# Optimization experiments

Measured on AMD Instinct MI355X. Metric: run time of the kernel, lower is better.

Reference implementation:

```python
import jax, jax.numpy as jnp
import numpy as np

NUM_KNNS = 200
TEMPERATURE = 0.07
NUM_CLASSES = 1000


def setup_inputs() -> dict:
    key = jax.random.key(0)
    k1, k2, k3, k4 = jax.random.split(key, 4)
    N, D, K = 1024, 512, 65536
    # features and queue are L2-normalized (queue init is normal_l2)
    features = jax.random.normal(k1, (N, D), jnp.float32)
    features = features / jnp.linalg.norm(features, axis=-1, keepdims=True)
    queue_features = jax.random.normal(k2, (K, D), jnp.float32)
    queue_features = queue_features / jnp.linalg.norm(queue_features, axis=-1, keepdims=True)
    labels = jax.random.randint(k3, (N,), 0, NUM_CLASSES, dtype=jnp.int32)
    queue_labels = jax.random.randint(k4, (K,), 0, NUM_CLASSES, dtype=jnp.int32)
    return {
        "features": features,
        "queue_features": queue_features,
        "labels": labels,
        "queue_labels": queue_labels,
        "queue_ptr": 0,
    }


def reference(features, queue_features, labels, queue_labels, queue_ptr):
    # --- kNN accuracy ---
    # similarity matmul: [N, K]
    sim = jnp.einsum('nd,kd->nk', features, queue_features)
    sim_weight, sim_indices = jax.lax.top_k(sim, k=NUM_KNNS)  # [N, k]
    sim_weight = jnp.exp(sim_weight / TEMPERATURE)
    # gather neighbor labels (equivalent to the one-hot einsum in the original)
    sim_labels = queue_labels[sim_indices]  # [N, k] int32
    one_hot_labels = jax.nn.one_hot(sim_labels, NUM_CLASSES, dtype=sim_weight.dtype)  # [N, k, C]
    pred_scores = jnp.sum(one_hot_labels * sim_weight[..., None], axis=1)  # [N, C]
    pred_labels = jnp.argmax(pred_scores, axis=-1)
    accuracy = jnp.mean((pred_labels == labels).astype(jnp.float32))

    # --- circular queue scatter update ---
    N = features.shape[0]
    K = queue_features.shape[0]
    inds = jnp.arange(N) + queue_ptr
    new_queue_features = queue_features.at[inds].set(features)
    new_queue_labels = queue_labels.at[inds].set(labels)
    new_queue_ptr = (queue_ptr + N) % K
    return accuracy, new_queue_features, new_queue_labels, new_queue_ptr
```

## Files before the change

kernel.cpp:

```cpp
#include <hip/hip_runtime.h>
#include <math.h>

#define N_ROWS 1024
#define DIM    512
#define KQ     65536
#define KNN    200
#define NCLS   1000
#define NBINS  4096
#define CAP    2048
#define INV_T  14.285714285714286f

typedef unsigned short u16;
typedef __attribute__((ext_vector_type(8))) short short8;
typedef __attribute__((ext_vector_type(4))) float f32x4;
struct alignas(8) U16x4 { u16 x, y, z, w; };

#define GLOAD_LDS16(g, l)                                               \
    __builtin_amdgcn_global_load_lds(                                   \
        (__attribute__((address_space(1))) void*)(g),                   \
        (__attribute__((address_space(3))) void*)(l), 16, 0, 0)

__device__ __forceinline__ void split1(float x, u16& h, u16& l) {
    unsigned u = __float_as_uint(x);
    unsigned hr = (u + 0x7FFFu + ((u >> 16) & 1u)) >> 16;
    float hf = __uint_as_float(hr << 16);
    float lo = x - hf;
    unsigned ul = __float_as_uint(lo);
    unsigned lr = (ul + 0x7FFFu + ((ul >> 16) & 1u)) >> 16;
    h = (u16)hr; l = (u16)lr;
}

#define QF_BLOCKS (KQ * DIM / 4 / 256)
#define FT_BLOCKS (N_ROWS * DIM / 4 / 256)

__global__ __launch_bounds__(256) void fused_update_split_kernel(
    const float* __restrict__ feats, const float* __restrict__ qf,
    const int* __restrict__ labels, const int* __restrict__ ql,
    const int* __restrict__ qptr,
    float* __restrict__ out_qf, float* __restrict__ out_ql,
    float* __restrict__ out_ptr,
    u16* __restrict__ Bhi, u16* __restrict__ Blo,
    u16* __restrict__ Ahi, u16* __restrict__ Alo) {
    int ptr = qptr[0];
    int b = blockIdx.x;
    if (b < QF_BLOCKS) {
        size_t t = (size_t)b * 256 + threadIdx.x;
        size_t idx = t * 4;
        int row = (int)(idx >> 9);
        int col = (int)(idx & 511);
        float4 v = *(const float4*)(qf + idx);
        U16x4 h, l;
        split1(v.x, h.x, l.x); split1(v.y, h.y, l.y);
        split1(v.z, h.z, l.z); split1(v.w, h.w, l.w);
        *(U16x4*)(Bhi + idx) = h;
        *(U16x4*)(Blo + idx) = l;
        int d = row - ptr; if (d < 0) d += KQ;
        float4 o = (d < N_ROWS) ? *(const float4*)(feats + (size_t)d * DIM + col) : v;
        *(float4*)(out_qf + idx) = o;
        if (col == 0)
            out_ql[row] = (float)((d < N_ROWS) ? labels[d] : ql[row]);
    } else {
        size_t t = (size_t)(b - QF_BLOCKS) * 256 + threadIdx.x;
        size_t idx = t * 4;
        float4 v = *(const float4*)(feats + idx);
        U16x4 h, l;
        split1(v.x, h.x, l.x); split1(v.y, h.y, l.y);
        split1(v.z, h.z, l.z); split1(v.w, h.w, l.w);
        *(U16x4*)(Ahi + idx) = h;
        *(U16x4*)(Alo + idx) = l;
        if (t == 0) out_ptr[0] = (float)((ptr + N_ROWS) % KQ);
    }
}

__global__ __launch_bounds__(256, 4) void gemm_mfma_kernel(
    const u16* __restrict__ Ahi, const u16* __restrict__ Alo,
    const u16* __restrict__ Bhi, const u16* __restrict__ Blo,
    float* __restrict__ C) {
    __shared__ u16 sA[2][128 * 32];
    __shared__ u16 sB[2][128 * 32];

    int tid = threadIdx.x;
    int wave = tid >> 6, lane = tid & 63;
    int q = lane >> 4, r = lane & 15;
    int bn = blockIdx.x, bm = blockIdx.y;
    int wm = wave & 1, wn = wave >> 1;

    const u16* gplane = (wave == 0) ? Ahi : (wave == 1) ? Alo
                      : (wave == 2) ? Bhi : Blo;
    int prow0 = (wave < 2) ? bm * 128 : bn * 128;
    const u16* gbase = gplane + (size_t)prow0 * DIM;
    u16* lbase = (wave == 0) ? sA[0] : (wave == 1) ? sA[1]
               : (wave == 2) ? sB[0] : sB[1];
    int lrow = lane >> 2;
    int lchunk = lane & 3;

    f32x4 acc[4][4] = {};

    for (int kt = 0; kt < DIM; kt += 32) {
        __syncthreads();
#pragma unroll
        for (int s = 0; s < 8; ++s) {
            const u16* g = gbase + (size_t)(s * 16 + lrow) * DIM + kt + lchunk * 8;
            GLOAD_LDS16(g, lbase + s * 512);
        }
        __syncthreads();

        short8 fa[2][4], fb[2][4];
#pragma unroll
        for (int t = 0; t < 4; ++t) {
            int am = wm * 64 + t * 16 + r;
            fa[0][t] = *(const short8*)&sA[0][am * 32 + q * 8];
            fa[1][t] = *(const short8*)&sA[1][am * 32 + q * 8];
            int bn_ = wn * 64 + t * 16 + r;
            fb[0][t] = *(const short8*)&sB[0][bn_ * 32 + q * 8];
            fb[1][t] = *(const short8*)&sB[1][bn_ * 32 + q * 8];
        }
#pragma unroll
        for (int i = 0; i < 4; ++i)
#pragma unroll
            for (int j = 0; j < 4; ++j) {
                acc[i][j] = __builtin_amdgcn_mfma_f32_16x16x32_bf16(
                    fa[0][i], fb[0][j], acc[i][j], 0, 0, 0);
                acc[i][j] = __builtin_amdgcn_mfma_f32_16x16x32_bf16(
                    fa[0][i], fb[1][j], acc[i][j], 0, 0, 0);
                acc[i][j] = __builtin_amdgcn_mfma_f32_16x16x32_bf16(
                    fa[1][i], fb[0][j], acc[i][j], 0, 0, 0);
            }
    }

#pragma unroll
    for (int i = 0; i < 4; ++i)
#pragma unroll
        for (int j = 0; j < 4; ++j)
#pragma unroll
            for (int g = 0; g < 4; ++g) {
                int row = bm * 128 + wm * 64 + i * 16 + q * 4 + g;
                int col = bn * 128 + wn * 64 + j * 16 + r;
                C[(size_t)row * KQ + col] = acc[i][j][g];
            }
}

#define LSTR 68
#define LA(k, m) ((k) * LSTR + (m))

__global__ __launch_bounds__(256) void gemm_nt_kernel(
    const float* __restrict__ A, const float* __restrict__ B,
    float* __restrict__ C) {
    __shared__ float As[32 * LSTR];
    __shared__ float Bs[32 * LSTR];
    int tid = threadIdx.x;
    int bn = blockIdx.x, bm = blockIdx.y;
    int tx = tid & 15, ty = tid >> 4;
    int lm = tid >> 3;
    int lk = (tid & 7) * 4;
    const float* Ab = A + (size_t)bm * 64 * DIM;
    const float* Bb = B + (size_t)bn * 64 * DIM;
    float acc[4][4] = {};
    for (int kt = 0; kt < DIM; kt += 32) {
        float4 a0 = *(const float4*)(Ab + (size_t)lm * DIM + kt + lk);
        float4 a1 = *(const float4*)(Ab + (size_t)(lm + 32) * DIM + kt + lk);
        float4 b0 = *(const float4*)(Bb + (size_t)lm * DIM + kt + lk);
        float4 b1 = *(const float4*)(Bb + (size_t)(lm + 32) * DIM + kt + lk);
        __syncthreads();
        As[LA(lk + 0, lm)] = a0.x;  As[LA(lk + 1, lm)] = a0.y;
        As[LA(lk + 2, lm)] = a0.z;  As[LA(lk + 3, lm)] = a0.w;
        As[LA(lk + 0, lm + 32)] = a1.x;  As[LA(lk + 1, lm + 32)] = a1.y;
        As[LA(lk + 2, lm + 32)] = a1.z;  As[LA(lk + 3, lm + 32)] = a1.w;
        Bs[LA(lk + 0, lm)] = b0.x;  Bs[LA(lk + 1, lm)] = b0.y;
        Bs[LA(lk + 2, lm)] = b0.z;  Bs[LA(lk + 3, lm)] = b0.w;
        Bs[LA(lk + 0, lm + 32)] = b1.x;  Bs[LA(lk + 1, lm + 32)] = b1.y;
        Bs[LA(lk + 2, lm + 32)] = b1.z;  Bs[LA(lk + 3, lm + 32)] = b1.w;
        __syncthreads();
#pragma unroll
        for (int kk = 0; kk < 32; ++kk) {
            float4 av = *(const float4*)&As[LA(kk, ty * 4)];
            float4 bv = *(const float4*)&Bs[LA(kk, tx * 4)];
            float a_[4] = {av.x, av.y, av.z, av.w};
            float b_[4] = {bv.x, bv.y, bv.z, bv.w};
#pragma unroll
            for (int i = 0; i < 4; ++i)
#pragma unroll
                for (int j = 0; j < 4; ++j) acc[i][j] += a_[i] * b_[j];
        }
    }
    for (int i = 0; i < 4; ++i) {
        float4 o = make_float4(acc[i][0], acc[i][1], acc[i][2], acc[i][3]);
        *(float4*)(C + (size_t)(bm * 64 + ty * 4 + i) * KQ + bn * 64 + tx * 4) = o;
    }
}

__device__ __forceinline__ unsigned order_key(float v) {
    unsigned u = __float_as_uint(v);
    return u ^ ((u & 0x80000000u) ? 0xFFFFFFFFu : 0x80000000u);
}

__global__ __launch_bounds__(1024) void topk_kernel(
    const float* __restrict__ sim, int r0,
    const int* __restrict__ ql, const int* __restrict__ labels,
    float* __restrict__ flags) {
    __shared__ unsigned hist[NBINS];
    __shared__ unsigned psum[1024];
    __shared__ float cval[CAP];
    __shared__ int   cidx[CAP];
    __shared__ float scores[NCLS];
    __shared__ float rbest[1024];
    __shared__ int   rcls[1024];
    __shared__ int   s_bstar, s_ncand;

    int row = blockIdx.x;
    int tid = threadIdx.x;
    const float4* s4 = (const float4*)(sim + (size_t)row * KQ);

    hist[tid] = 0; hist[tid + 1024] = 0; hist[tid + 2048] = 0; hist[tid + 3072] = 0;
    if (tid == 0) s_ncand = 0;
    __syncthreads();

    for (int i4 = tid; i4 < KQ / 4; i4 += 1024) {
        float4 v = s4[i4];
        atomicAdd(&hist[order_key(v.x) >> 20], 1u);
        atomicAdd(&hist[order_key(v.y) >> 20], 1u);
        atomicAdd(&hist[order_key(v.z) >> 20], 1u);
        atomicAdd(&hist[order_key(v.w) >> 20], 1u);
    }
    __syncthreads();

    unsigned loc = hist[4 * tid] + hist[4 * tid + 1] +
                   hist[4 * tid + 2] + hist[4 * tid + 3];
    psum[tid] = loc;
    __syncthreads();
    for (int off = 1; off < 1024; off <<= 1) {
        unsigned add = (tid + off < 1024) ? psum[tid + off] : 0u;
        __syncthreads();
        psum[tid] += add;
        __syncthreads();
    }
    unsigned running = psum[tid] - loc;
    for (int j = 3; j >= 0; --j) {
        unsigned c = hist[4 * tid + j];
        if (running < KNN && running + c >= KNN) s_bstar = 4 * tid + j;
        running += c;
    }
    __syncthreads();
    int bstar = s_bstar;

    for (int i4 = tid; i4 < KQ / 4; i4 += 1024) {
        float4 v = s4[i4];
        float vv[4] = {v.x, v.y, v.z, v.w};
#pragma unroll
        for (int c = 0; c < 4; ++c) {
            if ((int)(order_key(vv[c]) >> 20) >= bstar) {
                int p = atomicAdd(&s_ncand, 1);
                if (p < CAP) { cval[p] = vv[c]; cidx[p] = i4 * 4 + c; }
            }
        }
    }
    if (tid < NCLS) scores[tid] = 0.f;
    __syncthreads();

    int M = s_ncand; if (M > CAP) M = CAP;
    for (int c = tid; c < M; c += 1024) {
        float v = cval[c]; int id = cidx[c];
        int rank = 0;
        for (int j = 0; j < M; ++j) {
            float vj = cval[j];
            if (vj > v || (vj == v && cidx[j] < id)) rank++;
        }
        if (rank < KNN) {
            float w = expf(v * INV_T);
            atomicAdd(&scores[ql[id]], w);
        }
    }
    __syncthreads();

    float best = -1.f; int bc = 0;
    if (tid < NCLS) { best = scores[tid]; bc = tid; }
    rbest[tid] = best; rcls[tid] = bc;
    __syncthreads();
    for (int off = 512; off; off >>= 1) {
        if (tid < off) {
            float ob = rbest[tid + off]; int oc = rcls[tid + off];
            if (ob > rbest[tid] || (ob == rbest[tid] && oc < rcls[tid])) {
                rbest[tid] = ob; rcls[tid] = oc;
            }
        }
        __syncthreads();
    }
    if (tid == 0)
        flags[r0 + row] = (rcls[0] == labels[r0 + row]) ? 1.0f : 0.0f;
}

__global__ __launch_bounds__(256) void acc_kernel(
    const float* __restrict__ flags, float* __restrict__ out) {
    __shared__ float r[256];
    int tid = threadIdx.x;
    r[tid] = flags[tid] + flags[tid + 256] + flags[tid + 512] + flags[tid + 768];
    __syncthreads();
    for (int off = 128; off; off >>= 1) {
        if (tid < off) r[tid] += r[tid + off];
        __syncthreads();
    }
    if (tid == 0) out[0] = r[0] * (1.0f / 1024.0f);
}

extern "C" void kernel_launch(void* const* d_in, const int* in_sizes, int n_in,
                              void* d_out, int out_size, void* d_ws, size_t ws_size,
                              hipStream_t stream) {
    const float* feats  = (const float*)d_in[0];
    const float* qf     = (const float*)d_in[1];
    const int*   labels = (const int*)d_in[2];
    const int*   ql     = (const int*)d_in[3];
    const int*   qptr   = (const int*)d_in[4];

    float* out     = (float*)d_out;
    float* out_qf  = out + 1;
    float* out_ql  = out_qf + (size_t)KQ * DIM;
    float* out_ptr = out_ql + KQ;

    const size_t bplane = (size_t)KQ * DIM;
    const size_t aplane = (size_t)N_ROWS * DIM;

    int CH = 0;
    for (int c = 256; c >= 128; c >>= 1) {
        size_t need = 2 * bplane * 2 + 2 * aplane * 2 +
                      (size_t)c * KQ * 4 + N_ROWS * 4;
        if (need <= ws_size) { CH = c; break; }
    }

    if (CH > 0) {
        u16* Bhi = (u16*)d_ws;
        u16* Blo = Bhi + bplane;
        u16* Ahi = Blo + bplane;
        u16* Alo = Ahi + aplane;
        float* sim   = (float*)(Alo + aplane);
        float* flags = sim + (size_t)CH * KQ;

        fused_update_split_kernel<<<QF_BLOCKS + FT_BLOCKS, 256, 0, stream>>>(
            feats, qf, labels, ql, qptr, out_qf, out_ql, out_ptr,
            Bhi, Blo, Ahi, Alo);

        int nchunks = N_ROWS / CH;
        for (int c = 0; c < nchunks; ++c) {
            dim3 g(KQ / 128, CH / 128);
            gemm_mfma_kernel<<<g, 256, 0, stream>>>(
                Ahi + (size_t)c * CH * DIM, Alo + (size_t)c * CH * DIM,
                Bhi, Blo, sim);
            topk_kernel<<<CH, 1024, 0, stream>>>(sim, c * CH, ql, labels, flags);
        }
        acc_kernel<<<1, 256, 0, stream>>>(flags, out);
    } else {
        int CHf = 256;
        while (CHf > 64 &&
               ((size_t)CHf * KQ * sizeof(float) + N_ROWS * sizeof(float)) > ws_size)
            CHf >>= 1;
        float* sim   = (float*)d_ws;
        float* flags = (float*)((char*)d_ws + (size_t)CHf * KQ * sizeof(float));
        fused_update_split_kernel<<<QF_BLOCKS + FT_BLOCKS, 256, 0, stream>>>(
            feats, qf, labels, ql, qptr, out_qf, out_ql, out_ptr,
            (u16*)sim, (u16*)sim, (u16*)sim, (u16*)sim);
        int nchunks = N_ROWS / CHf;
        for (int c = 0; c < nchunks; ++c) {
            const float* A = feats + (size_t)c * CHf * DIM;
            dim3 g(KQ / 64, CHf / 64);
            gemm_nt_kernel<<<g, 256, 0, stream>>>(A, qf, sim);
            topk_kernel<<<CHf, 1024, 0, stream>>>(sim, c * CHf, ql, labels, flags);
        }
        acc_kernel<<<1, 256, 0, stream>>>(flags, out);
    }
}
```

Baseline: 669.5 us.

## Add 256x256-tile split-bf16 MFMA GEMM with ping-pong LDS staging and priority scheduling

Adds a new GEMM kernel for the split-bf16 (hi/lo) similarity matmul that uses 256x256 output tiles with 512 threads and 8 waves. It double-buffers LDS via direct global-to-LDS loads, interleaves fragment loads and MFMA groups with barriers and s_setprio, and walks 24 k-steps covering the three hi/lo plane products. The goal is more data reuse per LDS load and better overlap of memory with MFMA than the 128x128 kernel. It only runs when the chunk size is 256, and the large register and LDS footprint could limit occupancy.

After: 611.9 us. -8.6%, faster.

```diff
diff --git a/kernel.cpp b/kernel.cpp
--- a/kernel.cpp
+++ b/kernel.cpp
@@ -72,6 +72,129 @@
     }
 }
 
+#define NKT 24
+
+#define STAGE8(kt_, dA, dB)                                                    \
+  {                                                                            \
+    const u16* Ap_ = ((kt_) < 16) ? Ahi : Alo;                                 \
+    const u16* Bp_ = (((kt_) >> 3) == 1) ? Blo : Bhi;                          \
+    int ke_ = ((kt_) & 7) << 6;                                                \
+    const u16* ga_ = Ap_ + (size_t)(r0A + srow) * DIM + ke_ + scol;            \
+    const u16* gb_ = Bp_ + (size_t)(r0B + srow) * DIM + ke_ + scol;            \
+    GLOAD_LDS16(ga_ + (size_t)(8 * w0) * DIM,         &dA[0][w0 * 512]);       \
+    GLOAD_LDS16(ga_ + (size_t)(8 * w1) * DIM,         &dA[0][w1 * 512]);       \
+    GLOAD_LDS16(ga_ + (size_t)(128 + 8 * w0) * DIM,   &dA[1][w0 * 512]);       \
+    GLOAD_LDS16(ga_ + (size_t)(128 + 8 * w1) * DIM,   &dA[1][w1 * 512]);       \
+    GLOAD_LDS16(gb_ + (size_t)(8 * w0) * DIM,         &dB[0][w0 * 512]);       \
+    GLOAD_LDS16(gb_ + (size_t)(8 * w1) * DIM,         &dB[0][w1 * 512]);       \
+    GLOAD_LDS16(gb_ + (size_t)(128 + 8 * w0) * DIM,   &dB[1][w0 * 512]);       \
+    GLOAD_LDS16(gb_ + (size_t)(128 + 8 * w1) * DIM,   &dB[1][w1 * 512]);       \
+  }
+
+#define MM(t_, u_)                                                             \
+  acc[t_][u_] = __builtin_amdgcn_mfma_f32_16x16x32_bf16(                       \
+      fa[(t_) & 3][0], fb[u_][0], acc[t_][u_], 0, 0, 0);                       \
+  acc[t_][u_] = __builtin_amdgcn_mfma_f32_16x16x32_bf16(                       \
+      fa[(t_) & 3][1], fb[u_][1], acc[t_][u_], 0, 0, 0);
+
+#define TILE(kt_, RA, RB, SA, SB, DO_STAGE)                                    \
+  {                                                                            \
+    asm volatile("s_waitcnt vmcnt(0)" ::: "memory");                           \
+    __builtin_amdgcn_s_barrier();                                              \
+    const u16* aH_ = &RA[wm][0];                                               \
+    const u16* bH_ = &RB[wn >> 1][bB];                                         \
+                                                                  \
+    _Pragma("unroll") for (int t = 0; t < 4; ++t) {                            \
+      fa[t][0] = *(const short8*)(aH_ + t * 1024 + aoff + c0);                 \
+      fa[t][1] = *(const short8*)(aH_ + t * 1024 + aoff + c1);                 \
+    }                                                                          \
+    _Pragma("unroll") for (int u = 0; u < 2; ++u) {                            \
+      fb[u][0] = *(const short8*)(bH_ + u * 1024 + aoff + c0);                 \
+      fb[u][1] = *(const short8*)(bH_ + u * 1024 + aoff + c1);                 \
+    }                                                                          \
+    if (DO_STAGE) STAGE8((kt_) + 1, SA, SB);                                   \
+    __builtin_amdgcn_s_barrier();                                              \
+    __builtin_amdgcn_s_setprio(1);                                             \
+    _Pragma("unroll") for (int t = 0; t < 4; ++t) {                            \
+      MM(t, 0); MM(t, 1);                                                      \
+    }                                                                          \
+    __builtin_amdgcn_s_setprio(0);                                             \
+    __builtin_amdgcn_s_barrier();                                              \
+                                                                  \
+    _Pragma("unroll") for (int u = 2; u < 4; ++u) {                            \
+      fb[u][0] = *(const short8*)(bH_ + u * 1024 + aoff + c0);                 \
+      fb[u][1] = *(const short8*)(bH_ + u * 1024 + aoff + c1);                 \
+    }                                                                          \
+    __builtin_amdgcn_s_barrier();                                              \
+    __builtin_amdgcn_s_setprio(1);                                             \
+    _Pragma("unroll") for (int t = 0; t < 4; ++t) {                            \
+      MM(t, 2); MM(t, 3);                                                      \
+    }                                                                          \
+    __builtin_amdgcn_s_setprio(0);                                             \
+    __builtin_amdgcn_s_barrier();                                              \
+                                                                  \
+    _Pragma("unroll") for (int t = 0; t < 4; ++t) {                            \
+      fa[t][0] = *(const short8*)(aH_ + (t + 4) * 1024 + aoff + c0);           \
+      fa[t][1] = *(const short8*)(aH_ + (t + 4) * 1024 + aoff + c1);           \
+    }                                                                          \
+    __builtin_amdgcn_s_barrier();                                              \
+    __builtin_amdgcn_s_setprio(1);                                             \
+    _Pragma("unroll") for (int t = 4; t < 8; ++t) {                            \
+      MM(t, 2); MM(t, 3);                                                      \
+    }                                                                          \
+    __builtin_amdgcn_s_setprio(0);                                             \
+    __builtin_amdgcn_s_barrier();                                              \
+                                                                  \
+    __builtin_amdgcn_s_setprio(1);                                             \
+    _Pragma("unroll") for (int t = 4; t < 8; ++t) {                            \
+      MM(t, 0); MM(t, 1);                                                      \
+    }                                                                          \
+    __builtin_amdgcn_s_setprio(0);                                             \
+  }
+
+__global__ __launch_bounds__(512, 2) void gemm256_kernel(
+    const u16* __restrict__ Ahi, const u16* __restrict__ Alo,
+    const u16* __restrict__ Bhi, const u16* __restrict__ Blo,
+    float* __restrict__ C) {
+    __shared__ u16 sA0[2][8192], sB0[2][8192];
+    __shared__ u16 sA1[2][8192], sB1[2][8192];
+
+    int tid = threadIdx.x;
+    int wv = tid >> 6, lane = tid & 63;
+    int r = lane & 15, q = lane >> 4;
+    int wm = wv >> 2, wn = wv & 3;
+    int srow = lane >> 3;
+    int scol = ((lane & 7) ^ (lane >> 3)) << 3;
+    int w0 = wv, w1 = wv + 8;
+    int aoff = r << 6;
+    int c0 = (q << 3) ^ ((r & 7) << 3);
+    int c1 = (32 | (q << 3)) ^ ((r & 7) << 3);
+    int bB = (wn & 1) << 12;
+    int r0A = blockIdx.y << 8;
+    int r0B = blockIdx.x << 8;
+
+    f32x4 acc[8][4] = {};
+    short8 fa[4][2], fb[4][2];
+
+    STAGE8(0, sA0, sB0);
+
+    for (int kt = 0; kt < NKT; kt += 2) {
+        TILE(kt,     sA0, sB0, sA1, sB1, 1);
+        TILE(kt + 1, sA1, sB1, sA0, sB0, (kt + 2) < NKT);
+    }
+
+#pragma unroll
+    for (int t = 0; t < 8; ++t)
+#pragma unroll
+        for (int u = 0; u < 4; ++u)
+#pragma unroll
+            for (int g = 0; g < 4; ++g) {
+                int row = r0A + wm * 128 + t * 16 + q * 4 + g;
+                int col = r0B + wn * 64 + u * 16 + r;
+                C[(size_t)row * KQ + col] = acc[t][u][g];
+            }
+}
+
 __global__ __launch_bounds__(256, 4) void gemm_mfma_kernel(
     const u16* __restrict__ Ahi, const u16* __restrict__ Alo,
     const u16* __restrict__ Bhi, const u16* __restrict__ Blo,
@@ -340,10 +463,17 @@
 
         int nchunks = N_ROWS / CH;
         for (int c = 0; c < nchunks; ++c) {
-            dim3 g(KQ / 128, CH / 128);
-            gemm_mfma_kernel<<<g, 256, 0, stream>>>(
-                Ahi + (size_t)c * CH * DIM, Alo + (size_t)c * CH * DIM,
-                Bhi, Blo, sim);
+            if (CH == 256) {
+                dim3 g(KQ / 256, CH / 256);
+                gemm256_kernel<<<g, 512, 0, stream>>>(
+                    Ahi + (size_t)c * CH * DIM, Alo + (size_t)c * CH * DIM,
+                    Bhi, Blo, sim);
+            } else {
+                dim3 g(KQ / 128, CH / 128);
+                gemm_mfma_kernel<<<g, 256, 0, stream>>>(
+                    Ahi + (size_t)c * CH * DIM, Alo + (size_t)c * CH * DIM,
+                    Bhi, Blo, sim);
+            }
             topk_kernel<<<CH, 1024, 0, stream>>>(sim, c * CH, ql, labels, flags);
         }
         acc_kernel<<<1, 256, 0, stream>>>(flags, out);
```
